# Kernel optimization log

Measured on AMD Instinct MI355X. Metric: run time of the kernel, lower is better.

## Reference

```python
import jax, jax.numpy as jnp
import numpy as np

B, T, DM, H = 2, 2048, 1024, 16
D = DM // H
EPS = 1e-12  # torch F.normalize eps


def setup_inputs() -> dict:
    key = jax.random.key(0)
    ks = jax.random.split(key, 10)
    x = jax.random.normal(ks[0], (B, T, DM), dtype=jnp.float32)
    # causal additive mask, broadcastable to [B,H,T,T]
    causal = jnp.tril(jnp.ones((T, T), dtype=bool))
    mask = jnp.where(causal, 0.0, -1e9).astype(jnp.float32)[None, None]
    s = 0.02
    Wq = jax.random.normal(ks[1], (DM, DM), jnp.float32) * s
    Wk = jax.random.normal(ks[2], (DM, DM), jnp.float32) * s
    Wv = jax.random.normal(ks[3], (DM, DM), jnp.float32) * s
    Wo = jax.random.normal(ks[4], (DM, DM), jnp.float32) * s
    bq = jnp.zeros((DM,), jnp.float32)
    bk = jnp.zeros((DM,), jnp.float32)
    bv = jnp.zeros((DM,), jnp.float32)
    bo = jnp.zeros((DM,), jnp.float32)
    tau = jnp.full((H, 1, 1), 20.0, dtype=jnp.float32)
    return {"x": x, "mask": mask, "Wq": Wq, "bq": bq, "Wk": Wk, "bk": bk,
            "Wv": Wv, "bv": bv, "Wo": Wo, "bo": bo, "tau": tau}


def _l2norm(t):
    n = jnp.sqrt(jnp.sum(t * t, axis=-1, keepdims=True))
    return t / jnp.maximum(n, EPS)


def reference(x, mask, Wq, bq, Wk, bk, Wv, bv, Wo, bo, tau):
    Bz, Tz, _ = x.shape
    # projections (torch Linear: y = x @ W.T + b), split heads -> [B,H,T,D]
    q = (x @ Wq.T + bq).reshape(Bz, Tz, H, D).transpose(0, 2, 1, 3)
    k = (x @ Wk.T + bk).reshape(Bz, Tz, H, D).transpose(0, 2, 1, 3)
    v = (x @ Wv.T + bv).reshape(Bz, Tz, H, D).transpose(0, 2, 1, 3)
    q = _l2norm(q)
    k = _l2norm(k)
    # cosine-sim scores scaled by per-head learnable tau
    attn = jnp.einsum('bhqd,bhkd->bhqk', q, k) * tau[None]  # [B,H,T,T]
    attn = attn + mask
    attn = jax.nn.softmax(attn, axis=-1)
    out = jnp.einsum('bhqk,bhkd->bhqd', attn, v)
    out = out.transpose(0, 2, 1, 3).reshape(Bz, Tz, DM)
    return out @ Wo.T + bo
```

## Files before the change

### kernel.cpp

```cpp
#include <hip/hip_runtime.h>
#include <hip/hip_bf16.h>
#include <cstdint>

#define BB 2
#define TT 2048
#define DMo 1024
#define NH 16
#define HD 64
#define NR (BB*TT)

typedef __attribute__((ext_vector_type(8))) short bf16x8;
typedef __attribute__((ext_vector_type(4))) float f32x4;
typedef __attribute__((ext_vector_type(16))) float f32x16;
typedef __attribute__((ext_vector_type(4))) unsigned short u16x4;

static __device__ __forceinline__ float bf2f(unsigned short u) {
    union { unsigned int u32; float f; } x; x.u32 = ((unsigned int)u) << 16; return x.f;
}
static __device__ __forceinline__ unsigned short f2bf(float f) {
    union { float f; unsigned int u; } x; x.f = f;
    unsigned int r = x.u + 0x7fffu + ((x.u >> 16) & 1u);
    return (unsigned short)(r >> 16);
}
static __device__ __forceinline__ unsigned int cvtpk(float lo, float hi) {
    unsigned int r;
    asm("v_cvt_pk_bf16_f32 %0, %1, %2" : "=v"(r) : "v"(lo), "v"(hi));
    return r;
}

static __device__ __forceinline__ void gload16(const unsigned short* g, unsigned short* l) {
    __builtin_amdgcn_global_load_lds((const __attribute__((address_space(1))) void*)g,
                                     (__attribute__((address_space(3))) void*)l, 16, 0, 0);
}

__global__ void cvt_all(const float* __restrict__ x, const float* __restrict__ wq,
                        const float* __restrict__ wk, const float* __restrict__ wv,
                        const float* __restrict__ wo,
                        unsigned short* __restrict__ xb, unsigned short* __restrict__ wqb,
                        unsigned short* __restrict__ wkb, unsigned short* __restrict__ wvb,
                        unsigned short* __restrict__ wob) {
    int bi = blockIdx.x;
    const float* src; unsigned short* dst; int base;
    if (bi < 2048)      { src = x;  dst = xb;  base = 0; }
    else if (bi < 2560) { src = wq; dst = wqb; base = 2048; }
    else if (bi < 3072) { src = wk; dst = wkb; base = 2560; }
    else if (bi < 3584) { src = wv; dst = wvb; base = 3072; }
    else                { src = wo; dst = wob; base = 3584; }
    size_t i = (size_t)(bi - base) * 256 + threadIdx.x;
    const float4* p = reinterpret_cast<const float4*>(src) + 2 * i;
    float4 a = p[0], b = p[1];
    bf16x8 o;
    o[0] = (short)f2bf(a.x); o[1] = (short)f2bf(a.y); o[2] = (short)f2bf(a.z); o[3] = (short)f2bf(a.w);
    o[4] = (short)f2bf(b.x); o[5] = (short)f2bf(b.y); o[6] = (short)f2bf(b.z); o[7] = (short)f2bf(b.w);
    *(reinterpret_cast<bf16x8*>(dst) + i) = o;
}

__global__ __launch_bounds__(512, 4) void gemm_qkv(
    const unsigned short* __restrict__ A,
    const unsigned short* __restrict__ Wq,
    const unsigned short* __restrict__ Wk,
    const unsigned short* __restrict__ Wv,
    const float* __restrict__ bq, const float* __restrict__ bk, const float* __restrict__ bv,
    const float* __restrict__ tau,
    unsigned short* __restrict__ Qb, unsigned short* __restrict__ Kb,
    unsigned short* __restrict__ Vtb)
{
    __shared__ unsigned short lA[2][128 * 32];
    __shared__ unsigned short lB[2][256 * 32];
    const int K = DMo;
    int tid = threadIdx.x, lane = tid & 63, wid = tid >> 6;
    int l15 = lane & 15, l4 = lane >> 4;
    int wr = wid >> 2, wc = wid & 3;
    int bm = blockIdx.y, bn2 = blockIdx.x;
    int sel = bn2 >> 2, pn = bn2 & 3;
    const unsigned short* W = (sel == 0) ? Wq : ((sel == 1) ? Wk : Wv);
    const float* bias = (sel == 0) ? bq : ((sel == 1) ? bk : bv);
    f32x4 acc[4][4] = {};
    int srA = tid >> 2;
    int g8A = ((tid & 3) ^ (srA & 3)) * 8;
    const unsigned short* Ar = A + (size_t)(bm * 128 + srA) * K + g8A;
    int srB = tid >> 2;
    int g8B = ((tid & 3) ^ (srB & 3)) * 8;
    const unsigned short* Br0 = W + (size_t)(pn * 256 + srB) * K + g8B;
    const unsigned short* Br1 = Br0 + (size_t)128 * K;
    unsigned short* lA0 = lA[0] + tid * 8;
    unsigned short* lA1 = lA[1] + tid * 8;
    unsigned short* lB0a = lB[0] + tid * 8;
    unsigned short* lB0b = lB[0] + (tid + 512) * 8;
    unsigned short* lB1a = lB[1] + tid * 8;
    unsigned short* lB1b = lB[1] + (tid + 512) * 8;
    int cs = (l4 ^ (l15 & 3)) * 8;
    for (int k0 = 0; k0 < K; k0 += 64) {
        gload16(Ar + k0,       lA0);
        gload16(Ar + k0 + 32,  lA1);
        gload16(Br0 + k0,      lB0a);
        gload16(Br1 + k0,      lB0b);
        gload16(Br0 + k0 + 32, lB1a);
        gload16(Br1 + k0 + 32, lB1b);
        __syncthreads();
#pragma unroll
        for (int kk = 0; kk < 2; ++kk) {
            bf16x8 af[4], bfr[4];
#pragma unroll
            for (int m = 0; m < 4; ++m) af[m]  = *(const bf16x8*)(lA[kk] + (wr * 64 + m * 16 + l15) * 32 + cs);
#pragma unroll
            for (int n = 0; n < 4; ++n) bfr[n] = *(const bf16x8*)(lB[kk] + (wc * 64 + n * 16 + l15) * 32 + cs);
#pragma unroll
            for (int m = 0; m < 4; ++m)
#pragma unroll
                for (int n = 0; n < 4; ++n)
                    acc[m][n] = __builtin_amdgcn_mfma_f32_16x16x32_bf16(af[m], bfr[n], acc[m][n], 0, 0, 0);
        }
        __syncthreads();
    }
    float bz[4];
#pragma unroll
    for (int n = 0; n < 4; ++n) bz[n] = bias[pn * 256 + wc * 64 + n * 16 + l15];
    if (sel < 2) {
        unsigned short* Ob = (sel == 0) ? Qb : Kb;
        float tscale = (sel == 0) ? tau[pn * 4 + wc] : 1.0f;
#pragma unroll
        for (int m = 0; m < 4; ++m) {
            int row = bm * 128 + wr * 64 + m * 16 + l4 * 4;
#pragma unroll
            for (int i = 0; i < 4; ++i) {
                float v[4]; float ss = 0.f;
#pragma unroll
                for (int n = 0; n < 4; ++n) { v[n] = acc[m][n][i] + bz[n]; ss += v[n] * v[n]; }
#pragma unroll
                for (int off = 1; off < 16; off <<= 1) ss += __shfl_xor(ss, off);
                float sc = tscale / fmaxf(sqrtf(ss), 1e-12f);
#pragma unroll
                for (int n = 0; n < 4; ++n)
                    Ob[(size_t)(row + i) * DMo + pn * 256 + wc * 64 + n * 16 + l15] = f2bf(v[n] * sc);
            }
        }
    } else {
#pragma unroll
        for (int m = 0; m < 4; ++m) {
            int row = bm * 128 + wr * 64 + m * 16 + l4 * 4;
#pragma unroll
            for (int n = 0; n < 4; ++n) {
                int col = pn * 256 + wc * 64 + n * 16 + l15;
                u16x4 pk;
#pragma unroll
                for (int i = 0; i < 4; ++i) pk[i] = f2bf(acc[m][n][i] + bz[n]);
                int b = row >> 11, t = row & 2047;
                int bh = b * NH + (col >> 6), d = col & 63;
                *reinterpret_cast<u16x4*>(Vtb + ((size_t)bh * HD + d) * TT + t) = pk;
            }
        }
    }
}

__global__ __launch_bounds__(256) void gemm_out(
    const unsigned short* __restrict__ A,
    const unsigned short* __restrict__ Bm,
    const float* __restrict__ bias,
    float* __restrict__ Cout)
{
    __shared__ unsigned short lA[2][128 * 32];
    __shared__ unsigned short lB[2][128 * 32];
    const int K = DMo, N = DMo;
    int tid = threadIdx.x, lane = tid & 63, wid = tid >> 6;
    int l15 = lane & 15, l4 = lane >> 4;
    int wr = wid >> 1, wc = wid & 1;
    int lid = blockIdx.x;
    int xcd = lid & 7, idx = lid >> 3;
    int bn = idx % 8;
    int bm = (idx / 8) * 8 + xcd;
    f32x4 acc[4][4] = {};
    int sr = tid >> 2;
    int g8 = ((tid & 3) ^ (sr & 3)) * 8;
    const unsigned short* Ar0 = A + (size_t)(bm * 128 + sr) * K + g8;
    const unsigned short* Ar1 = Ar0 + (size_t)64 * K;
    const unsigned short* Br0 = Bm + (size_t)(bn * 128 + sr) * K + g8;
    const unsigned short* Br1 = Br0 + (size_t)64 * K;
    unsigned short* lA0 = lA[0] + tid * 8;
    unsigned short* lA1 = lA[1] + tid * 8;
    unsigned short* lB0 = lB[0] + tid * 8;
    unsigned short* lB1 = lB[1] + tid * 8;
    int cs = (l4 ^ (l15 & 3)) * 8;
    for (int k0 = 0; k0 < K; k0 += 64) {
        gload16(Ar0 + k0,      lA0);
        gload16(Ar1 + k0,      lA0 + 2048);
        gload16(Ar0 + k0 + 32, lA1);
        gload16(Ar1 + k0 + 32, lA1 + 2048);
        gload16(Br0 + k0,      lB0);
        gload16(Br1 + k0,      lB0 + 2048);
        gload16(Br0 + k0 + 32, lB1);
        gload16(Br1 + k0 + 32, lB1 + 2048);
        __syncthreads();
#pragma unroll
        for (int kk = 0; kk < 2; ++kk) {
            bf16x8 af[4], bfr[4];
#pragma unroll
            for (int m = 0; m < 4; ++m) af[m]  = *(const bf16x8*)(lA[kk] + (wr * 64 + m * 16 + l15) * 32 + cs);
#pragma unroll
            for (int n = 0; n < 4; ++n) bfr[n] = *(const bf16x8*)(lB[kk] + (wc * 64 + n * 16 + l15) * 32 + cs);
#pragma unroll
            for (int m = 0; m < 4; ++m)
#pragma unroll
                for (int n = 0; n < 4; ++n)
                    acc[m][n] = __builtin_amdgcn_mfma_f32_16x16x32_bf16(af[m], bfr[n], acc[m][n], 0, 0, 0);
        }
        __syncthreads();
    }
#pragma unroll
    for (int m = 0; m < 4; ++m) {
        int row = bm * 128 + wr * 64 + m * 16 + l4 * 4;
#pragma unroll
        for (int n = 0; n < 4; ++n) {
            int col = bn * 128 + wc * 64 + n * 16 + l15;
            float bz = bias[col];
#pragma unroll
            for (int i = 0; i < 4; ++i)
                Cout[(size_t)(row + i) * N + col] = acc[m][n][i] + bz;
        }
    }
}

__global__ __launch_bounds__(256, 2) void attn_fwd(
    const unsigned short* __restrict__ Qn,
    const unsigned short* __restrict__ Kn,
    const unsigned short* __restrict__ Vt,
    const float* __restrict__ tau,
    unsigned short* __restrict__ Out)
{
    __shared__ unsigned short lK[2][64][68];
    __shared__ unsigned short lVt[2][64][68];
    __shared__ float lInv[4][32];
    int bid = blockIdx.x;
    int xcd = bid & 7, r = bid >> 3;
    int bh = ((r & 3) << 3) + xcd;
    int jid = r >> 2;
    int qb = (jid < 8) ? (15 - jid) : (jid - 8);
    int b = bh >> 4, h = bh & 15;
    int q0 = qb * 128;
    int nt = 2 * qb + 2;
    int tid = threadIdx.x, lane = tid & 63, wid = tid >> 6;
    int l31 = lane & 31, half = lane >> 5;
    float M = fabsf(tau[h]);

    const unsigned short* Kg = Kn + (size_t)b * TT * DMo + h * HD;
    const unsigned short* Vg = Vt + (size_t)bh * HD * TT;

    int rA = tid >> 3, gA = (tid & 7) * 8;

    size_t qoff = ((size_t)b * TT + q0 + wid * 32 + l31) * DMo + h * HD;
    bf16x8 qf[4];
#pragma unroll
    for (int ks = 0; ks < 4; ++ks)
        qf[ks] = *(const bf16x8*)(Qn + qoff + ks * 16 + half * 8);

    f32x16 accO[2] = {};
    float l_run = 0.f;

    bf16x8 rk0, rk1, rv0, rv1;
    rk0 = *(const bf16x8*)(Kg + (size_t)rA * DMo + gA);
    rk1 = *(const bf16x8*)(Kg + (size_t)(rA + 32) * DMo + gA);
    rv0 = *(const bf16x8*)(Vg + (size_t)rA * TT + gA);
    rv1 = *(const bf16x8*)(Vg + (size_t)(rA + 32) * TT + gA);
    *reinterpret_cast<bf16x8*>(&lK[0][rA][gA])       = rk0;
    *reinterpret_cast<bf16x8*>(&lK[0][rA + 32][gA])  = rk1;
    *reinterpret_cast<bf16x8*>(&lVt[0][rA][gA])      = rv0;
    *reinterpret_cast<bf16x8*>(&lVt[0][rA + 32][gA]) = rv1;
    if (nt > 1) {
        rk0 = *(const bf16x8*)(Kg + (size_t)(64 + rA) * DMo + gA);
        rk1 = *(const bf16x8*)(Kg + (size_t)(64 + rA + 32) * DMo + gA);
        rv0 = *(const bf16x8*)(Vg + (size_t)rA * TT + 64 + gA);
        rv1 = *(const bf16x8*)(Vg + (size_t)(rA + 32) * TT + 64 + gA);
    }

    for (int j = 0; j < nt; ++j) {
        int cur = j & 1;
        __syncthreads();
        if (j + 1 < nt) {
            *reinterpret_cast<bf16x8*>(&lK[cur ^ 1][rA][gA])       = rk0;
            *reinterpret_cast<bf16x8*>(&lK[cur ^ 1][rA + 32][gA])  = rk1;
            *reinterpret_cast<bf16x8*>(&lVt[cur ^ 1][rA][gA])      = rv0;
            *reinterpret_cast<bf16x8*>(&lVt[cur ^ 1][rA + 32][gA]) = rv1;
            if (j + 2 < nt) {
                rk0 = *(const bf16x8*)(Kg + (size_t)((j + 2) * 64 + rA) * DMo + gA);
                rk1 = *(const bf16x8*)(Kg + (size_t)((j + 2) * 64 + rA + 32) * DMo + gA);
                rv0 = *(const bf16x8*)(Vg + (size_t)rA * TT + (j + 2) * 64 + gA);
                rv1 = *(const bf16x8*)(Vg + (size_t)(rA + 32) * TT + (j + 2) * 64 + gA);
            }
        }
        f32x16 s[2] = {};
        __builtin_amdgcn_s_setprio(1);
#pragma unroll
        for (int kvb = 0; kvb < 2; ++kvb)
#pragma unroll
            for (int ks = 0; ks < 4; ++ks) {
                bf16x8 a = *(const bf16x8*)(&lK[cur][kvb * 32 + l31][ks * 16 + half * 8]);
                s[kvb] = __builtin_amdgcn_mfma_f32_32x32x16_bf16(a, qf[ks], s[kvb], 0, 0, 0);
            }
        __builtin_amdgcn_s_setprio(0);
        if (j >= nt - 2) {
            int qg = q0 + wid * 32 + l31;
#pragma unroll
            for (int kvb = 0; kvb < 2; ++kvb)
#pragma unroll
                for (int rr = 0; rr < 16; ++rr) {
                    int kvg = j * 64 + kvb * 32 + (rr & 3) + 8 * (rr >> 2) + 4 * half;
                    if (kvg > qg) s[kvb][rr] = -1e30f;
                }
        }
        float rs = 0.f;
#pragma unroll
        for (int kvb = 0; kvb < 2; ++kvb)
#pragma unroll
            for (int rr = 0; rr < 16; ++rr) {
                float p = __expf(s[kvb][rr] - M); s[kvb][rr] = p; rs += p;
            }
        l_run += rs;
        unsigned int Wp[2][4][2];
#pragma unroll
        for (int kvb = 0; kvb < 2; ++kvb)
#pragma unroll
            for (int jj = 0; jj < 4; ++jj)
#pragma unroll
                for (int t = 0; t < 2; ++t)
                    Wp[kvb][jj][t] = cvtpk(s[kvb][4 * jj + 2 * t], s[kvb][4 * jj + 2 * t + 1]);
        bf16x8 pa[4];
#pragma unroll
        for (int kvs = 0; kvs < 4; ++kvs) {
            int c = kvs >> 1, d0 = 2 * (kvs & 1), d1 = d0 + 1;
            unsigned int A0 = half ? Wp[c][d1][0] : Wp[c][d0][0];
            unsigned int A1 = half ? Wp[c][d1][1] : Wp[c][d0][1];
            unsigned int B0 = half ? Wp[c][d0][0] : Wp[c][d1][0];
            unsigned int B1 = half ? Wp[c][d0][1] : Wp[c][d1][1];
            unsigned int x0 = B0, y0 = B0, x1 = B1, y1 = B1;
            asm volatile("v_permlane32_swap_b32 %0, %1" : "+v"(x0), "+v"(y0));
            asm volatile("v_permlane32_swap_b32 %0, %1" : "+v"(x1), "+v"(y1));
            unsigned int P0 = half ? x0 : y0;
            unsigned int P1 = half ? x1 : y1;
            unsigned int paw[4];
            paw[0] = half ? P0 : A0;
            paw[1] = half ? P1 : A1;
            paw[2] = half ? A0 : P0;
            paw[3] = half ? A1 : P1;
            pa[kvs] = *reinterpret_cast<bf16x8*>(paw);
        }
        __builtin_amdgcn_s_setprio(1);
#pragma unroll
        for (int dblk = 0; dblk < 2; ++dblk)
#pragma unroll
            for (int kvs = 0; kvs < 4; ++kvs) {
                bf16x8 bv = *(const bf16x8*)(&lVt[cur][dblk * 32 + l31][kvs * 16 + half * 8]);
                accO[dblk] = __builtin_amdgcn_mfma_f32_32x32x16_bf16(pa[kvs], bv, accO[dblk], 0, 0, 0);
            }
        __builtin_amdgcn_s_setprio(0);
    }
    l_run += __shfl_xor(l_run, 32);
    float inv = 1.0f / l_run;
    lInv[wid][l31] = inv;
    asm volatile("s_waitcnt lgkmcnt(0)" ::: "memory");
    __builtin_amdgcn_sched_barrier(0);
#pragma unroll
    for (int rr = 0; rr < 16; ++rr) {
        int qrow = (rr & 3) + 8 * (rr >> 2) + 4 * half;
        float iv = lInv[wid][qrow];
        size_t rowoff = (size_t)(b * TT + q0 + wid * 32 + qrow) * DMo + h * HD + l31;
#pragma unroll
        for (int dblk = 0; dblk < 2; ++dblk)
            Out[rowoff + dblk * 32] = f2bf(accO[dblk][rr] * iv);
    }
}

extern "C" void kernel_launch(void* const* d_in, const int* in_sizes, int n_in,
                              void* d_out, int out_size, void* d_ws, size_t ws_size,
                              hipStream_t stream) {
    const float* x   = (const float*)d_in[0];
    const float* Wq  = (const float*)d_in[2];
    const float* bq  = (const float*)d_in[3];
    const float* Wk  = (const float*)d_in[4];
    const float* bk  = (const float*)d_in[5];
    const float* Wv  = (const float*)d_in[6];
    const float* bv  = (const float*)d_in[7];
    const float* Wo  = (const float*)d_in[8];
    const float* bo  = (const float*)d_in[9];
    const float* tau = (const float*)d_in[10];

    char* ws = (char*)d_ws;
    unsigned short* xb  = (unsigned short*)(ws);
    unsigned short* Wqb = (unsigned short*)(ws + ((size_t)8  << 20));
    unsigned short* Wkb = (unsigned short*)(ws + ((size_t)10 << 20));
    unsigned short* Wvb = (unsigned short*)(ws + ((size_t)12 << 20));
    unsigned short* Wob = (unsigned short*)(ws + ((size_t)14 << 20));
    unsigned short* Qb  = (unsigned short*)(ws + ((size_t)16 << 20));
    unsigned short* Kb  = (unsigned short*)(ws + ((size_t)24 << 20));
    unsigned short* Vtb = (unsigned short*)(ws + ((size_t)32 << 20));
    unsigned short* AOb = (unsigned short*)(ws + ((size_t)40 << 20));

    cvt_all<<<4096, 256, 0, stream>>>(x, Wq, Wk, Wv, Wo, xb, Wqb, Wkb, Wvb, Wob);

    gemm_qkv<<<dim3(12, NR / 128), 512, 0, stream>>>(xb, Wqb, Wkb, Wvb, bq, bk, bv,
                                                     tau, Qb, Kb, Vtb);

    attn_fwd<<<512, 256, 0, stream>>>(Qb, Kb, Vtb, tau, AOb);

    gemm_out<<<256, 256, 0, stream>>>(AOb, Wob, bo, (float*)d_out);
}
```

Measured before the change: 107.9 us.

## Split KV tiles across two wave groups and pair causal q-blocks per block

The attention kernel now runs 512-thread blocks. Two groups of four waves each take alternating 64-wide KV tiles for the same 128 query rows, then combine their partial outputs and row sums through shared memory. Each block handles two query blocks in turn: one long causal block (15-jid) and one short one (jid). This evens out work per block and halves the grid to 256 blocks. In exchange it costs more LDS (a combine buffer plus doubled K/V staging), extra barriers, and a serial final normalize done by only half the waves.

```diff
diff --git a/kernel.cpp b/kernel.cpp
--- a/kernel.cpp
+++ b/kernel.cpp
@@ -220,25 +220,24 @@
     }
 }
 
-__global__ __launch_bounds__(256, 2) void attn_fwd(
+__global__ __launch_bounds__(512, 1) void attn_fwd(
     const unsigned short* __restrict__ Qn,
     const unsigned short* __restrict__ Kn,
     const unsigned short* __restrict__ Vt,
     const float* __restrict__ tau,
     unsigned short* __restrict__ Out)
 {
-    __shared__ unsigned short lK[2][64][68];
-    __shared__ unsigned short lVt[2][64][68];
+    __shared__ unsigned short lK[2][2][64][68];
+    __shared__ unsigned short lVt[2][2][64][68];
+    __shared__ float lX[4][64][34];
     __shared__ float lInv[4][32];
     int bid = blockIdx.x;
     int xcd = bid & 7, r = bid >> 3;
     int bh = ((r & 3) << 3) + xcd;
     int jid = r >> 2;
-    int qb = (jid < 8) ? (15 - jid) : (jid - 8);
     int b = bh >> 4, h = bh & 15;
-    int q0 = qb * 128;
-    int nt = 2 * qb + 2;
     int tid = threadIdx.x, lane = tid & 63, wid = tid >> 6;
+    int grp = wid >> 2, w4 = wid & 3;
     int l31 = lane & 31, half = lane >> 5;
     float M = fabsf(tau[h]);
 
@@ -247,125 +246,144 @@
 
     int rA = tid >> 3, gA = (tid & 7) * 8;
 
-    size_t qoff = ((size_t)b * TT + q0 + wid * 32 + l31) * DMo + h * HD;
-    bf16x8 qf[4];
-#pragma unroll
-    for (int ks = 0; ks < 4; ++ks)
-        qf[ks] = *(const bf16x8*)(Qn + qoff + ks * 16 + half * 8);
-
-    f32x16 accO[2] = {};
-    float l_run = 0.f;
-
-    bf16x8 rk0, rk1, rv0, rv1;
-    rk0 = *(const bf16x8*)(Kg + (size_t)rA * DMo + gA);
-    rk1 = *(const bf16x8*)(Kg + (size_t)(rA + 32) * DMo + gA);
-    rv0 = *(const bf16x8*)(Vg + (size_t)rA * TT + gA);
-    rv1 = *(const bf16x8*)(Vg + (size_t)(rA + 32) * TT + gA);
-    *reinterpret_cast<bf16x8*>(&lK[0][rA][gA])       = rk0;
-    *reinterpret_cast<bf16x8*>(&lK[0][rA + 32][gA])  = rk1;
-    *reinterpret_cast<bf16x8*>(&lVt[0][rA][gA])      = rv0;
-    *reinterpret_cast<bf16x8*>(&lVt[0][rA + 32][gA]) = rv1;
-    if (nt > 1) {
-        rk0 = *(const bf16x8*)(Kg + (size_t)(64 + rA) * DMo + gA);
-        rk1 = *(const bf16x8*)(Kg + (size_t)(64 + rA + 32) * DMo + gA);
-        rv0 = *(const bf16x8*)(Vg + (size_t)rA * TT + 64 + gA);
-        rv1 = *(const bf16x8*)(Vg + (size_t)(rA + 32) * TT + 64 + gA);
-    }
-
-    for (int j = 0; j < nt; ++j) {
-        int cur = j & 1;
+    for (int ph = 0; ph < 2; ++ph) {
+        int qb = ph ? jid : (15 - jid);
+        int q0 = qb * 128;
+        int nt = 2 * qb + 2;
+        int nh2 = nt >> 1;
+
+        size_t qoff = ((size_t)b * TT + q0 + w4 * 32 + l31) * DMo + h * HD;
+        bf16x8 qf[4];
+#pragma unroll
+        for (int ks = 0; ks < 4; ++ks)
+            qf[ks] = *(const bf16x8*)(Qn + qoff + ks * 16 + half * 8);
+
+        f32x16 accO[2] = {};
+        float l_run = 0.f;
+
+        bf16x8 rk0, rk1, rv0, rv1;
+        auto ldpair = [&](int jp) {
+            rk0 = *(const bf16x8*)(Kg + (size_t)(2 * jp * 64 + rA) * DMo + gA);
+            rk1 = *(const bf16x8*)(Kg + (size_t)((2 * jp + 1) * 64 + rA) * DMo + gA);
+            rv0 = *(const bf16x8*)(Vg + (size_t)rA * TT + 2 * jp * 64 + gA);
+            rv1 = *(const bf16x8*)(Vg + (size_t)rA * TT + (2 * jp + 1) * 64 + gA);
+        };
+        auto stpair = [&](int pb) {
+            *reinterpret_cast<bf16x8*>(&lK[pb][0][rA][gA])  = rk0;
+            *reinterpret_cast<bf16x8*>(&lK[pb][1][rA][gA])  = rk1;
+            *reinterpret_cast<bf16x8*>(&lVt[pb][0][rA][gA]) = rv0;
+            *reinterpret_cast<bf16x8*>(&lVt[pb][1][rA][gA]) = rv1;
+        };
+        ldpair(0);
+        if (ph == 1) __syncthreads();
+        stpair(0);
+        if (nh2 > 1) ldpair(1);
+
+        for (int t2 = 0; t2 < nh2; ++t2) {
+            int cur = t2 & 1;
+            __syncthreads();
+            if (t2 + 1 < nh2) {
+                stpair(cur ^ 1);
+                if (t2 + 2 < nh2) ldpair(t2 + 2);
+            }
+            int j = 2 * t2 + grp;
+            f32x16 s[2] = {};
+            __builtin_amdgcn_s_setprio(1);
+#pragma unroll
+            for (int kvb = 0; kvb < 2; ++kvb)
+#pragma unroll
+                for (int ks = 0; ks < 4; ++ks) {
+                    bf16x8 a = *(const bf16x8*)(&lK[cur][grp][kvb * 32 + l31][ks * 16 + half * 8]);
+                    s[kvb] = __builtin_amdgcn_mfma_f32_32x32x16_bf16(a, qf[ks], s[kvb], 0, 0, 0);
+                }
+            __builtin_amdgcn_s_setprio(0);
+            if (t2 == nh2 - 1) {
+                int qg = q0 + w4 * 32 + l31;
+#pragma unroll
+                for (int kvb = 0; kvb < 2; ++kvb)
+#pragma unroll
+                    for (int rr = 0; rr < 16; ++rr) {
+                        int kvg = j * 64 + kvb * 32 + (rr & 3) + 8 * (rr >> 2) + 4 * half;
+                        if (kvg > qg) s[kvb][rr] = -1e30f;
+                    }
+            }
+            float rs = 0.f;
+#pragma unroll
+            for (int kvb = 0; kvb < 2; ++kvb)
+#pragma unroll
+                for (int rr = 0; rr < 16; ++rr) {
+                    float p = __expf(s[kvb][rr] - M); s[kvb][rr] = p; rs += p;
+                }
+            l_run += rs;
+            unsigned int Wp[2][4][2];
+#pragma unroll
+            for (int kvb = 0; kvb < 2; ++kvb)
+#pragma unroll
+                for (int jj = 0; jj < 4; ++jj)
+#pragma unroll
+                    for (int t = 0; t < 2; ++t)
+                        Wp[kvb][jj][t] = cvtpk(s[kvb][4 * jj + 2 * t], s[kvb][4 * jj + 2 * t + 1]);
+            bf16x8 pa[4];
+#pragma unroll
+            for (int kvs = 0; kvs < 4; ++kvs) {
+                int c = kvs >> 1, d0 = 2 * (kvs & 1), d1 = d0 + 1;
+                unsigned int A0 = half ? Wp[c][d1][0] : Wp[c][d0][0];
+                unsigned int A1 = half ? Wp[c][d1][1] : Wp[c][d0][1];
+                unsigned int B0 = half ? Wp[c][d0][0] : Wp[c][d1][0];
+                unsigned int B1 = half ? Wp[c][d0][1] : Wp[c][d1][1];
+                unsigned int x0 = B0, y0 = B0, x1 = B1, y1 = B1;
+                asm volatile("v_permlane32_swap_b32 %0, %1" : "+v"(x0), "+v"(y0));
+                asm volatile("v_permlane32_swap_b32 %0, %1" : "+v"(x1), "+v"(y1));
+                unsigned int P0 = half ? x0 : y0;
+                unsigned int P1 = half ? x1 : y1;
+                unsigned int paw[4];
+                paw[0] = half ? P0 : A0;
+                paw[1] = half ? P1 : A1;
+                paw[2] = half ? A0 : P0;
+                paw[3] = half ? A1 : P1;
+                pa[kvs] = *reinterpret_cast<bf16x8*>(paw);
+            }
+            __builtin_amdgcn_s_setprio(1);
+#pragma unroll
+            for (int dblk = 0; dblk < 2; ++dblk)
+#pragma unroll
+                for (int kvs = 0; kvs < 4; ++kvs) {
+                    bf16x8 bv = *(const bf16x8*)(&lVt[cur][grp][dblk * 32 + l31][kvs * 16 + half * 8]);
+                    accO[dblk] = __builtin_amdgcn_mfma_f32_32x32x16_bf16(pa[kvs], bv, accO[dblk], 0, 0, 0);
+                }
+            __builtin_amdgcn_s_setprio(0);
+        }
+        l_run += __shfl_xor(l_run, 32);
+        if (grp == 1) {
+#pragma unroll
+            for (int dblk = 0; dblk < 2; ++dblk)
+#pragma unroll
+                for (int rr = 0; rr < 16; ++rr)
+                    lX[w4][lane][dblk * 16 + rr] = accO[dblk][rr];
+            if (lane < 32) lX[w4][lane][32] = l_run;
+        }
         __syncthreads();
-        if (j + 1 < nt) {
-            *reinterpret_cast<bf16x8*>(&lK[cur ^ 1][rA][gA])       = rk0;
-            *reinterpret_cast<bf16x8*>(&lK[cur ^ 1][rA + 32][gA])  = rk1;
-            *reinterpret_cast<bf16x8*>(&lVt[cur ^ 1][rA][gA])      = rv0;
-            *reinterpret_cast<bf16x8*>(&lVt[cur ^ 1][rA + 32][gA]) = rv1;
-            if (j + 2 < nt) {
-                rk0 = *(const bf16x8*)(Kg + (size_t)((j + 2) * 64 + rA) * DMo + gA);
-                rk1 = *(const bf16x8*)(Kg + (size_t)((j + 2) * 64 + rA + 32) * DMo + gA);
-                rv0 = *(const bf16x8*)(Vg + (size_t)rA * TT + (j + 2) * 64 + gA);
-                rv1 = *(const bf16x8*)(Vg + (size_t)(rA + 32) * TT + (j + 2) * 64 + gA);
-            }
-        }
-        f32x16 s[2] = {};
-        __builtin_amdgcn_s_setprio(1);
-#pragma unroll
-        for (int kvb = 0; kvb < 2; ++kvb)
-#pragma unroll
-            for (int ks = 0; ks < 4; ++ks) {
-                bf16x8 a = *(const bf16x8*)(&lK[cur][kvb * 32 + l31][ks * 16 + half * 8]);
-                s[kvb] = __builtin_amdgcn_mfma_f32_32x32x16_bf16(a, qf[ks], s[kvb], 0, 0, 0);
-            }
-        __builtin_amdgcn_s_setprio(0);
-        if (j >= nt - 2) {
-            int qg = q0 + wid * 32 + l31;
-#pragma unroll
-            for (int kvb = 0; kvb < 2; ++kvb)
-#pragma unroll
-                for (int rr = 0; rr < 16; ++rr) {
-                    int kvg = j * 64 + kvb * 32 + (rr & 3) + 8 * (rr >> 2) + 4 * half;
-                    if (kvg > qg) s[kvb][rr] = -1e30f;
-                }
-        }
-        float rs = 0.f;
-#pragma unroll
-        for (int kvb = 0; kvb < 2; ++kvb)
+        if (grp == 0) {
+#pragma unroll
+            for (int dblk = 0; dblk < 2; ++dblk)
+#pragma unroll
+                for (int rr = 0; rr < 16; ++rr)
+                    accO[dblk][rr] += lX[w4][lane][dblk * 16 + rr];
+            l_run += lX[w4][l31][32];
+            float inv = 1.0f / l_run;
+            if (lane < 32) lInv[w4][l31] = inv;
+            asm volatile("s_waitcnt lgkmcnt(0)" ::: "memory");
+            __builtin_amdgcn_sched_barrier(0);
 #pragma unroll
             for (int rr = 0; rr < 16; ++rr) {
-                float p = __expf(s[kvb][rr] - M); s[kvb][rr] = p; rs += p;
-            }
-        l_run += rs;
-        unsigned int Wp[2][4][2];
-#pragma unroll
-        for (int kvb = 0; kvb < 2; ++kvb)
-#pragma unroll
-            for (int jj = 0; jj < 4; ++jj)
-#pragma unroll
-                for (int t = 0; t < 2; ++t)
-                    Wp[kvb][jj][t] = cvtpk(s[kvb][4 * jj + 2 * t], s[kvb][4 * jj + 2 * t + 1]);
-        bf16x8 pa[4];
-#pragma unroll
-        for (int kvs = 0; kvs < 4; ++kvs) {
-            int c = kvs >> 1, d0 = 2 * (kvs & 1), d1 = d0 + 1;
-            unsigned int A0 = half ? Wp[c][d1][0] : Wp[c][d0][0];
-            unsigned int A1 = half ? Wp[c][d1][1] : Wp[c][d0][1];
-            unsigned int B0 = half ? Wp[c][d0][0] : Wp[c][d1][0];
-            unsigned int B1 = half ? Wp[c][d0][1] : Wp[c][d1][1];
-            unsigned int x0 = B0, y0 = B0, x1 = B1, y1 = B1;
-            asm volatile("v_permlane32_swap_b32 %0, %1" : "+v"(x0), "+v"(y0));
-            asm volatile("v_permlane32_swap_b32 %0, %1" : "+v"(x1), "+v"(y1));
-            unsigned int P0 = half ? x0 : y0;
-            unsigned int P1 = half ? x1 : y1;
-            unsigned int paw[4];
-            paw[0] = half ? P0 : A0;
-            paw[1] = half ? P1 : A1;
-            paw[2] = half ? A0 : P0;
-            paw[3] = half ? A1 : P1;
-            pa[kvs] = *reinterpret_cast<bf16x8*>(paw);
-        }
-        __builtin_amdgcn_s_setprio(1);
-#pragma unroll
-        for (int dblk = 0; dblk < 2; ++dblk)
-#pragma unroll
-            for (int kvs = 0; kvs < 4; ++kvs) {
-                bf16x8 bv = *(const bf16x8*)(&lVt[cur][dblk * 32 + l31][kvs * 16 + half * 8]);
-                accO[dblk] = __builtin_amdgcn_mfma_f32_32x32x16_bf16(pa[kvs], bv, accO[dblk], 0, 0, 0);
-            }
-        __builtin_amdgcn_s_setprio(0);
-    }
-    l_run += __shfl_xor(l_run, 32);
-    float inv = 1.0f / l_run;
-    lInv[wid][l31] = inv;
-    asm volatile("s_waitcnt lgkmcnt(0)" ::: "memory");
-    __builtin_amdgcn_sched_barrier(0);
-#pragma unroll
-    for (int rr = 0; rr < 16; ++rr) {
-        int qrow = (rr & 3) + 8 * (rr >> 2) + 4 * half;
-        float iv = lInv[wid][qrow];
-        size_t rowoff = (size_t)(b * TT + q0 + wid * 32 + qrow) * DMo + h * HD + l31;
-#pragma unroll
-        for (int dblk = 0; dblk < 2; ++dblk)
-            Out[rowoff + dblk * 32] = f2bf(accO[dblk][rr] * iv);
+                int qrow = (rr & 3) + 8 * (rr >> 2) + 4 * half;
+                float iv = lInv[w4][qrow];
+                size_t rowoff = (size_t)(b * TT + q0 + w4 * 32 + qrow) * DMo + h * HD + l31;
+#pragma unroll
+                for (int dblk = 0; dblk < 2; ++dblk)
+                    Out[rowoff + dblk * 32] = f2bf(accO[dblk][rr] * iv);
+            }
+        }
     }
 }
 
@@ -399,7 +417,7 @@
     gemm_qkv<<<dim3(12, NR / 128), 512, 0, stream>>>(xb, Wqb, Wkb, Wvb, bq, bk, bv,
                                                      tau, Qb, Kb, Vtb);
 
-    attn_fwd<<<512, 256, 0, stream>>>(Qb, Kb, Vtb, tau, AOb);
+    attn_fwd<<<256, 512, 0, stream>>>(Qb, Kb, Vtb, tau, AOb);
 
     gemm_out<<<256, 256, 0, stream>>>(AOb, Wob, bo, (float*)d_out);
 }
```

Measured after the change: 104.7 us. -3.0%, faster.
